# Kernel tuning notes

Hardware: AMD Instinct MI355X
Metric: run time of the kernel (lower is better)

Reference implementation:

```python
import jax, jax.numpy as jnp
import numpy as np

B, T = 32, 512
DA, DV = 1280, 768
D = DA + DV          # fused audio+video feature dim = 2048
DM = 256             # mamba d_model
L = 4                # n_layers
DI = 2 * DM          # d_inner (expand=2)
DS = 16              # d_state
DC = 4               # d_conv
R = DM // 16         # dt_rank = ceil(256/16)
H = 128              # attn-pool hidden
NC = 8               # emotion classes
EPS_TIN = 1e-5
EPS_LN = 1e-5


def _ln(x, g, b):
    mu = x.mean(-1, keepdims=True)
    v = ((x - mu) ** 2).mean(-1, keepdims=True)
    return (x - mu) / jnp.sqrt(v + EPS_LN) * g + b


def _mamba(u, in_w, cw, cb, xw, dtw, dtb, A_log, Dp, ow):
    # u: [B,T,DM] -> [B,T,DM]; Mamba(v1) selective scan, d_state=16, d_conv=4, expand=2
    xz = jnp.einsum('btd,ed->bte', u, in_w)            # [B,T,2*DI]
    x, z = xz[..., :DI], xz[..., DI:]
    xp = jnp.pad(x, ((0, 0), (DC - 1, 0), (0, 0)))     # causal depthwise conv1d
    xc = sum(xp[:, k:k + u.shape[1], :] * cw[:, k] for k in range(DC)) + cb
    x = jax.nn.silu(xc)
    dbc = jnp.einsum('btd,ed->bte', x, xw)             # [B,T,R+2*DS]
    dt = jax.nn.softplus(jnp.einsum('btr,dr->btd', dbc[..., :R], dtw) + dtb)
    Bm = dbc[..., R:R + DS]
    Cm = dbc[..., R + DS:]
    A = -jnp.exp(A_log)                                # [DI,DS]

    def step(h, inp):
        dt_t, B_t, C_t, x_t = inp                      # [B,DI],[B,DS],[B,DS],[B,DI]
        h = jnp.exp(dt_t[..., None] * A) * h + dt_t[..., None] * B_t[:, None, :] * x_t[..., None]
        return h, jnp.einsum('bds,bs->bd', h, C_t)

    h0 = jnp.zeros((u.shape[0], DI, DS), u.dtype)
    xs = (dt.swapaxes(0, 1), Bm.swapaxes(0, 1), Cm.swapaxes(0, 1), x.swapaxes(0, 1))
    _, ys = jax.lax.scan(step, h0, xs)
    y = ys.swapaxes(0, 1) + Dp * x
    y = y * jax.nn.silu(z)
    return jnp.einsum('bti,oi->bto', y, ow)


def _forward(x, tin_gamma, tin_beta, proj_w, proj_b, ln_g, ln_b, in_proj_w, conv_w, conv_b,
             x_proj_w, dt_proj_w, dt_proj_b, A_log, D_param, out_proj_w,
             out_ln_g, out_ln_b, res_scale, attn_w1, attn_b1, attn_w2, head_w, head_b, lengths):
    mask = jnp.arange(T)[None, :] < lengths[:, None]   # [B,T]
    m = mask[..., None].astype(x.dtype)
    # FusedTIN: masked temporal instance norm + affine
    denom = jnp.maximum(lengths, 1).astype(x.dtype)[:, None, None]
    mean = (x * m).sum(1, keepdims=True) / denom
    var = (((x - mean) ** 2) * m).sum(1, keepdims=True) / denom
    xn = (x - mean) / jnp.sqrt(var + EPS_TIN) * m
    xn = (xn * tin_gamma + tin_beta) * m
    # MambaStack: proj_in + prenorm residual mamba blocks (dropout = eval identity)
    h = jnp.einsum('btd,md->btm', xn, proj_w) + proj_b
    for l in range(L):
        y = _mamba(_ln(h, ln_g[l], ln_b[l]), in_proj_w[l], conv_w[l], conv_b[l],
                   x_proj_w[l], dt_proj_w[l], dt_proj_b[l], A_log[l], D_param[l], out_proj_w[l])
        h = h + res_scale * y
    h = _ln(h, out_ln_g, out_ln_b)
    # MaskedAttnPool
    s = jnp.einsum('bth,oh->bto', jnp.tanh(jnp.einsum('btd,hd->bth', h, attn_w1) + attn_b1), attn_w2)[..., 0]
    logits = jnp.where(mask, s, -jnp.inf)
    alpha = jnp.nan_to_num(jax.nn.softmax(logits, axis=1)) * mask
    alpha = alpha / jnp.clip(alpha.sum(1, keepdims=True), 1e-9)
    ctx = (alpha[..., None] * h).sum(1)
    # classifier head
    return jnp.einsum('bd,cd->bc', ctx, head_w) + head_b


def setup_inputs() -> dict:
    key = jax.random.key(0)
    ks = jax.random.split(key, 16)
    s = 0.05
    inp = {}
    inp['x'] = jax.random.normal(ks[0], (B, T, D), jnp.float32)
    inp['lengths'] = jax.random.randint(ks[1], (B,), T // 4, T + 1)
    inp['tin_gamma'] = jnp.ones((D,), jnp.float32)
    inp['tin_beta'] = jnp.zeros((D,), jnp.float32)
    inp['proj_w'] = jax.random.normal(ks[2], (DM, D), jnp.float32) * s
    inp['proj_b'] = jnp.zeros((DM,), jnp.float32)
    inp['ln_g'] = jnp.ones((L, DM), jnp.float32)
    inp['ln_b'] = jnp.zeros((L, DM), jnp.float32)
    inp['in_proj_w'] = jax.random.normal(ks[3], (L, 2 * DI, DM), jnp.float32) * s
    inp['conv_w'] = jax.random.normal(ks[4], (L, DI, DC), jnp.float32) * s
    inp['conv_b'] = jnp.zeros((L, DI), jnp.float32)
    inp['x_proj_w'] = jax.random.normal(ks[5], (L, R + 2 * DS, DI), jnp.float32) * s
    inp['dt_proj_w'] = jax.random.normal(ks[6], (L, DI, R), jnp.float32) * s
    inp['dt_proj_b'] = jnp.full((L, DI), -3.0, jnp.float32) + jax.random.normal(ks[7], (L, DI), jnp.float32) * 0.1
    inp['A_log'] = jnp.log(jnp.broadcast_to(jnp.arange(1, DS + 1, dtype=jnp.float32), (L, DI, DS)) + 0.0)
    inp['D_param'] = jnp.ones((L, DI), jnp.float32)
    inp['out_proj_w'] = jax.random.normal(ks[8], (L, DM, DI), jnp.float32) * s
    inp['out_ln_g'] = jnp.ones((DM,), jnp.float32)
    inp['out_ln_b'] = jnp.zeros((DM,), jnp.float32)
    inp['res_scale'] = jnp.asarray(0.1, jnp.float32)
    inp['attn_w1'] = jax.random.normal(ks[9], (H, DM), jnp.float32) * s
    inp['attn_b1'] = jnp.zeros((H,), jnp.float32)
    inp['attn_w2'] = jax.random.normal(ks[10], (1, H), jnp.float32) * s
    inp['head_w'] = jax.random.normal(ks[11], (NC, DM), jnp.float32) * s
    inp['head_b'] = jnp.zeros((NC,), jnp.float32)
    return inp


def reference(x, tin_gamma, tin_beta, proj_w, proj_b, ln_g, ln_b, in_proj_w, conv_w, conv_b,
              x_proj_w, dt_proj_w, dt_proj_b, A_log, D_param, out_proj_w,
              out_ln_g, out_ln_b, res_scale, attn_w1, attn_b1, attn_w2, head_w, head_b, lengths):
    return _forward(x, tin_gamma, tin_beta, proj_w, proj_b, ln_g, ln_b, in_proj_w, conv_w, conv_b,
                    x_proj_w, dt_proj_w, dt_proj_b, A_log, D_param, out_proj_w,
                    out_ln_g, out_ln_b, res_scale, attn_w1, attn_b1, attn_w2, head_w, head_b, lengths)
```

## Files before the change

kernel.cpp:

```cpp
#include <hip/hip_runtime.h>

#define NB 32
#define NT 512
#define ND 2048
#define NDM 256
#define NDI 512
#define NDS 16
#define NR 16
#define NH 128
#define NNC 8
#define NL 4
#define NM (NB*NT)

typedef __attribute__((ext_vector_type(8))) short short8;
typedef __attribute__((ext_vector_type(4))) float floatx4;

__device__ __forceinline__ unsigned short f2bf_rn(float f) {
    unsigned u = __builtin_bit_cast(unsigned, f);
    u += 0x7FFFu + ((u >> 16) & 1u);
    return (unsigned short)(u >> 16);
}
__device__ __forceinline__ void cvt8(const float* v, short8& h8, short8& l8) {
#pragma unroll
    for (int q = 0; q < 8; ++q) {
        unsigned short hb = f2bf_rn(v[q]);
        float hf = __builtin_bit_cast(float, (unsigned)hb << 16);
        h8[q] = (short)hb;
        l8[q] = (short)f2bf_rn(v[q] - hf);
    }
}
__device__ __forceinline__ float quad_sum(float v) {
    int i = __builtin_bit_cast(int, v);
    int j = __builtin_amdgcn_update_dpp(0, i, 0xB1, 0xF, 0xF, true);
    v += __builtin_bit_cast(float, j);
    i = __builtin_bit_cast(int, v);
    j = __builtin_amdgcn_update_dpp(0, i, 0x4E, 0xF, 0xF, true);
    v += __builtin_bit_cast(float, j);
    return v;
}

__global__ __launch_bounds__(256) void tin_stats_k(
    const float* __restrict__ x, const int* __restrict__ lengths,
    float* __restrict__ mean, float* __restrict__ rstd)
{
    __shared__ float rs_[4][64];
    __shared__ float rq_[4][64];
    const int b = blockIdx.x >> 5;
    const int d0 = (blockIdx.x & 31) << 6;
    const int dl = threadIdx.x & 63;
    const int strip = threadIdx.x >> 6;
    const int len = lengths[b];
    const int d = d0 + dl;
    float s = 0.f, q = 0.f;
    for (int t = strip; t < len; t += 4) {
        float v = x[((size_t)(b*NT + t))*ND + d];
        s += v; q += v*v;
    }
    rs_[strip][dl] = s; rq_[strip][dl] = q;
    __syncthreads();
    if (threadIdx.x < 64) {
        float S = rs_[0][dl]+rs_[1][dl]+rs_[2][dl]+rs_[3][dl];
        float Q = rq_[0][dl]+rq_[1][dl]+rq_[2][dl]+rq_[3][dl];
        float inv = 1.f / (float)(len < 1 ? 1 : len);
        float mu = S * inv;
        float var = Q * inv - mu*mu;
        mean[b*ND + d] = mu;
        rstd[b*ND + d] = rsqrtf(var + 1e-5f);
    }
}

#define SLN 264
__global__ __launch_bounds__(256) void tin_norm_k(
    const float* __restrict__ x, const int* __restrict__ lengths,
    const float* __restrict__ mean, const float* __restrict__ rstd,
    const float* __restrict__ g, const float* __restrict__ be,
    short* __restrict__ Oh, short* __restrict__ Ol)
{
    __shared__ float sT[16][SLN];
    const int tid = threadIdx.x;
    const int row = tid >> 4, c = tid & 15;
    const int m = blockIdx.x*16 + row;
    const int b = m >> 9, t = m & (NT-1);
    const int len = lengths[b];
    const int kg0 = blockIdx.y*256 + c*16;
    if (t >= len) {
#pragma unroll
        for (int i = 0; i < 16; ++i) sT[row][c*16 + i] = 0.f;
    } else {
#pragma unroll
        for (int qq = 0; qq < 4; ++qq) {
            const int kg = kg0 + qq*4;
            float4 v = *(const float4*)(x + (size_t)m*ND + kg);
            float4 mn = *(const float4*)(mean + b*ND + kg);
            float4 rr = *(const float4*)(rstd + b*ND + kg);
            float4 gg = *(const float4*)(g + kg);
            float4 bb = *(const float4*)(be + kg);
            sT[row][c*16+qq*4+0] = (v.x-mn.x)*rr.x*gg.x + bb.x;
            sT[row][c*16+qq*4+1] = (v.y-mn.y)*rr.y*gg.y + bb.y;
            sT[row][c*16+qq*4+2] = (v.z-mn.z)*rr.z*gg.z + bb.z;
            sT[row][c*16+qq*4+3] = (v.w-mn.w)*rr.w*gg.w + bb.w;
        }
    }
    __syncthreads();
#pragma unroll
    for (int q = 0; q < 2; ++q) {
        const int slot = tid + 256*q;
        const int tile = slot >> 6, ln2 = slot & 63;
        const int mr = ln2 & 15, kc = ln2 >> 4;
        float v[8];
        *(float4*)&v[0] = *(const float4*)&sT[mr][tile*32 + kc*8];
        *(float4*)&v[4] = *(const float4*)&sT[mr][tile*32 + kc*8 + 4];
        short8 h8, l8; cvt8(v, h8, l8);
        const size_t off = ((size_t)blockIdx.x*64 + blockIdx.y*8 + tile)*512 + ln2*8;
        *(short8*)(Oh + off) = h8;
        *(short8*)(Ol + off) = l8;
    }
}

__global__ __launch_bounds__(256) void wconv_k(
    const float* __restrict__ W, short* __restrict__ Oh, short* __restrict__ Ol,
    int K, int nmod, int nvalid)
{
    __shared__ float sT[16][SLN];
    const int tid = threadIdx.x;
    const int row = tid >> 4, c = tid & 15;
    const int n = blockIdx.x*16 + row;
    const int rr = n % nmod;
    const int kg0 = blockIdx.y*256 + c*16;
    if (rr >= nvalid) {
#pragma unroll
        for (int i = 0; i < 16; ++i) sT[row][c*16 + i] = 0.f;
    } else {
        const int src = (n/nmod)*nvalid + rr;
#pragma unroll
        for (int qq = 0; qq < 4; ++qq) {
            float4 v = *(const float4*)(W + (size_t)src*K + kg0 + qq*4);
            *(float4*)&sT[row][c*16+qq*4] = v;
        }
    }
    __syncthreads();
#pragma unroll
    for (int q = 0; q < 2; ++q) {
        const int slot = tid + 256*q;
        const int tile = slot >> 6, ln2 = slot & 63;
        const int mr = ln2 & 15, kc = ln2 >> 4;
        float v[8];
        *(float4*)&v[0] = *(const float4*)&sT[mr][tile*32 + kc*8];
        *(float4*)&v[4] = *(const float4*)&sT[mr][tile*32 + kc*8 + 4];
        short8 h8, l8; cvt8(v, h8, l8);
        const size_t off = ((size_t)blockIdx.x*(K>>5) + blockIdx.y*8 + tile)*512 + ln2*8;
        *(short8*)(Oh + off) = h8;
        *(short8*)(Ol + off) = l8;
    }
}

template<int MSUB, int NSUB, int EPI>
__global__ __launch_bounds__(256) void mgemm_k(
    const short* __restrict__ Ah, const short* __restrict__ Al,
    const short* __restrict__ Bh, const short* __restrict__ Bl,
    const float* __restrict__ bias, float* __restrict__ C,
    int ldc, int Nvalid, int K, const float* __restrict__ rsp)
{
    __shared__ __align__(16) short lds[(MSUB+NSUB)*1024];
    short* As_h = lds;
    short* As_l = lds + MSUB*512;
    short* Bs_h = lds + MSUB*1024;
    short* Bs_l = lds + MSUB*1024 + NSUB*512;
    const int tid = threadIdx.x, lane = tid & 63, w = tid >> 6;
    const int m0t = blockIdx.x * MSUB;
    const int n0t = blockIdx.y * NSUB;
    const int Ktiles = K >> 5;
    constexpr int MI = MSUB/2, NI = NSUB/2;
    constexpr int ASG = MSUB/4, BSG = NSUB/4;
    const int wm = w >> 1, wn = w & 1;

    floatx4 acc[MI][NI] = {};
    short8 rah[ASG], ral[ASG], rbh[BSG], rbl[BSG];

#pragma unroll
    for (int u = 0; u < ASG; ++u) {
        const size_t off = ((size_t)(m0t + w*ASG + u)*Ktiles)*512 + lane*8;
        rah[u] = *(const short8*)(Ah + off); ral[u] = *(const short8*)(Al + off);
    }
#pragma unroll
    for (int u = 0; u < BSG; ++u) {
        const size_t off = ((size_t)(n0t + w*BSG + u)*Ktiles)*512 + lane*8;
        rbh[u] = *(const short8*)(Bh + off); rbl[u] = *(const short8*)(Bl + off);
    }

    for (int kb = 0; kb < Ktiles; ++kb) {
        __syncthreads();
#pragma unroll
        for (int u = 0; u < ASG; ++u) {
            const int sub = w*ASG + u;
            *(short8*)&As_h[sub*512 + lane*8] = rah[u];
            *(short8*)&As_l[sub*512 + lane*8] = ral[u];
        }
#pragma unroll
        for (int u = 0; u < BSG; ++u) {
            const int sub = w*BSG + u;
            *(short8*)&Bs_h[sub*512 + lane*8] = rbh[u];
            *(short8*)&Bs_l[sub*512 + lane*8] = rbl[u];
        }
        __syncthreads();
        if (kb + 1 < Ktiles) {
#pragma unroll
            for (int u = 0; u < ASG; ++u) {
                const size_t off = ((size_t)(m0t + w*ASG + u)*Ktiles + kb + 1)*512 + lane*8;
                rah[u] = *(const short8*)(Ah + off); ral[u] = *(const short8*)(Al + off);
            }
#pragma unroll
            for (int u = 0; u < BSG; ++u) {
                const size_t off = ((size_t)(n0t + w*BSG + u)*Ktiles + kb + 1)*512 + lane*8;
                rbh[u] = *(const short8*)(Bh + off); rbl[u] = *(const short8*)(Bl + off);
            }
        }
        short8 fah[MI], fal[MI], fbh[NI], fbl[NI];
#pragma unroll
        for (int i = 0; i < MI; ++i) {
            const int sub = wm*MI + i;
            fah[i] = *(const short8*)&As_h[sub*512 + lane*8];
            fal[i] = *(const short8*)&As_l[sub*512 + lane*8];
        }
#pragma unroll
        for (int j = 0; j < NI; ++j) {
            const int sub = wn*NI + j;
            fbh[j] = *(const short8*)&Bs_h[sub*512 + lane*8];
            fbl[j] = *(const short8*)&Bs_l[sub*512 + lane*8];
        }
#pragma unroll
        for (int i = 0; i < MI; ++i)
#pragma unroll
            for (int j = 0; j < NI; ++j) {
                acc[i][j] = __builtin_amdgcn_mfma_f32_16x16x32_bf16(fah[i], fbh[j], acc[i][j], 0, 0, 0);
                acc[i][j] = __builtin_amdgcn_mfma_f32_16x16x32_bf16(fah[i], fbl[j], acc[i][j], 0, 0, 0);
                acc[i][j] = __builtin_amdgcn_mfma_f32_16x16x32_bf16(fal[i], fbh[j], acc[i][j], 0, 0, 0);
            }
    }

    const float rs = (EPI == 1) ? rsp[0] : 0.f;
    const int lc = lane >> 4, col = lane & 15;
#pragma unroll
    for (int j = 0; j < NI; ++j) {
        const int n = (n0t + wn*NI + j)*16 + col;
        if (n < Nvalid) {
            const float bv = (EPI != 1 && bias) ? bias[n] : 0.f;
#pragma unroll
            for (int i = 0; i < MI; ++i) {
                const int mb = (m0t + wm*MI + i)*16 + lc*4;
#pragma unroll
                for (int r = 0; r < 4; ++r) {
                    float v = acc[i][j][r];
                    float* cp = C + (size_t)(mb + r)*ldc + n;
                    if (EPI == 0)      *cp = v + bv;
                    else if (EPI == 1) *cp = fmaf(rs, v, *cp);
                    else               *cp = tanhf(v + bv);
                }
            }
        }
    }
}

template<int WF32>
__global__ __launch_bounds__(256) void ln_blk_k(
    const float* __restrict__ in, const float* __restrict__ g,
    const float* __restrict__ b,
    short* __restrict__ Oh, short* __restrict__ Ol, float* __restrict__ o32)
{
    __shared__ float sT[16][SLN];
    const int tid = threadIdx.x;
    const int row = tid >> 4, c = tid & 15;
    const int m = blockIdx.x*16 + row;
    float v[16];
#pragma unroll
    for (int qq = 0; qq < 4; ++qq)
        *(float4*)&v[qq*4] = *(const float4*)(in + (size_t)m*NDM + c*16 + qq*4);
    float s = 0.f, q = 0.f;
#pragma unroll
    for (int i = 0; i < 16; ++i) { s += v[i]; q += v[i]*v[i]; }
#pragma unroll
    for (int o = 8; o; o >>= 1) { s += __shfl_xor(s, o); q += __shfl_xor(q, o); }
    const float mu = s * (1.f/NDM);
    const float r = rsqrtf(q*(1.f/NDM) - mu*mu + 1e-5f);
#pragma unroll
    for (int i = 0; i < 16; ++i) {
        const int kg = c*16 + i;
        v[i] = (v[i]-mu)*r*g[kg] + b[kg];
        sT[row][kg] = v[i];
    }
    if (WF32) {
#pragma unroll
        for (int qq = 0; qq < 4; ++qq)
            *(float4*)(o32 + (size_t)m*NDM + c*16 + qq*4) = *(const float4*)&v[qq*4];
    }
    __syncthreads();
#pragma unroll
    for (int qv = 0; qv < 2; ++qv) {
        const int slot = tid + 256*qv;
        const int tile = slot >> 6, ln2 = slot & 63;
        const int mr = ln2 & 15, kc = ln2 >> 4;
        float vv[8];
        *(float4*)&vv[0] = *(const float4*)&sT[mr][tile*32 + kc*8];
        *(float4*)&vv[4] = *(const float4*)&sT[mr][tile*32 + kc*8 + 4];
        short8 h8, l8; cvt8(vv, h8, l8);
        const size_t off = ((size_t)blockIdx.x*8 + tile)*512 + ln2*8;
        *(short8*)(Oh + off) = h8;
        *(short8*)(Ol + off) = l8;
    }
}

#define SCV 520
__global__ __launch_bounds__(256) void conv_blk_k(
    const float* __restrict__ xz, const float* __restrict__ cw,
    const float* __restrict__ cb, float* __restrict__ xc32,
    short* __restrict__ Oh, short* __restrict__ Ol)
{
    __shared__ float sT[16][SCV];
    const int tid = threadIdx.x;
    const int row = tid >> 4, cg = tid & 15;
    const int m = blockIdx.x*16 + row;
    const int t = m & (NT-1);
#pragma unroll
    for (int grp = 0; grp < 4; ++grp) {
        const int ch = cg*32 + grp*8;
        float a[8];
        *(float4*)&a[0] = *(const float4*)(cb + ch);
        *(float4*)&a[4] = *(const float4*)(cb + ch + 4);
        float4 wv[8];
#pragma unroll
        for (int i = 0; i < 8; ++i) wv[i] = *(const float4*)(cw + (ch+i)*4);
#pragma unroll
        for (int kk = 0; kk < 4; ++kk) {
            if (t - 3 + kk >= 0) {
                const float* xp = xz + (size_t)(m-3+kk)*(2*NDI) + ch;
                float xv[8];
                *(float4*)&xv[0] = *(const float4*)xp;
                *(float4*)&xv[4] = *(const float4*)(xp + 4);
                const float tap[8] = {
                    kk==0?wv[0].x:kk==1?wv[0].y:kk==2?wv[0].z:wv[0].w,
                    kk==0?wv[1].x:kk==1?wv[1].y:kk==2?wv[1].z:wv[1].w,
                    kk==0?wv[2].x:kk==1?wv[2].y:kk==2?wv[2].z:wv[2].w,
                    kk==0?wv[3].x:kk==1?wv[3].y:kk==2?wv[3].z:wv[3].w,
                    kk==0?wv[4].x:kk==1?wv[4].y:kk==2?wv[4].z:wv[4].w,
                    kk==0?wv[5].x:kk==1?wv[5].y:kk==2?wv[5].z:wv[5].w,
                    kk==0?wv[6].x:kk==1?wv[6].y:kk==2?wv[6].z:wv[6].w,
                    kk==0?wv[7].x:kk==1?wv[7].y:kk==2?wv[7].z:wv[7].w};
#pragma unroll
                for (int i = 0; i < 8; ++i) a[i] = fmaf(xv[i], tap[i], a[i]);
            }
        }
#pragma unroll
        for (int i = 0; i < 8; ++i) a[i] = a[i] / (1.f + __expf(-a[i]));
        *(float4*)&sT[row][ch] = *(const float4*)&a[0];
        *(float4*)&sT[row][ch+4] = *(const float4*)&a[4];
        *(float4*)(xc32 + (size_t)m*NDI + ch) = *(const float4*)&a[0];
        *(float4*)(xc32 + (size_t)m*NDI + ch + 4) = *(const float4*)&a[4];
    }
    __syncthreads();
#pragma unroll
    for (int q = 0; q < 4; ++q) {
        const int slot = tid + 256*q;
        const int tile = slot >> 6, ln2 = slot & 63;
        const int mr = ln2 & 15, kc = ln2 >> 4;
        float vv[8];
        *(float4*)&vv[0] = *(const float4*)&sT[mr][tile*32 + kc*8];
        *(float4*)&vv[4] = *(const float4*)&sT[mr][tile*32 + kc*8 + 4];
        short8 h8, l8; cvt8(vv, h8, l8);
        const size_t off = ((size_t)blockIdx.x*16 + tile)*512 + ln2*8;
        *(short8*)(Oh + off) = h8;
        *(short8*)(Ol + off) = l8;
    }
}

__global__ __launch_bounds__(256) void dt_k(
    const float* __restrict__ dbc, const float* __restrict__ dtw,
    const float* __restrict__ dtb, float* __restrict__ dt)
{
    const int m = blockIdx.x;
    const float* rsrc = dbc + (size_t)m*48;
    float rv[16];
#pragma unroll
    for (int i = 0; i < 16; ++i) rv[i] = rsrc[i];
#pragma unroll
    for (int hh = 0; hh < 2; ++hh) {
        const int d = hh*256 + threadIdx.x;
        const float* wr = dtw + d*16;
        float a = dtb[d];
#pragma unroll
        for (int i = 0; i < 16; ++i) a = fmaf(rv[i], wr[i], a);
        dt[(size_t)m*NDI + d] = (a > 20.f) ? a : log1pf(__expf(a));
    }
}

__global__ __launch_bounds__(256) void scan_k(
    const float* __restrict__ dbc, const float* __restrict__ dtp,
    const float* __restrict__ xcp, const float* __restrict__ xz,
    const float* __restrict__ Alog, const float* __restrict__ Dp,
    short* __restrict__ Yh, short* __restrict__ Yl)
{
    __shared__ float sBC[64][32];
    __shared__ float sDt[64][68];
    __shared__ float sX[64][68];
    __shared__ float sY[64][68];
    const int tid = threadIdx.x;
    const int w = tid >> 6, lane = tid & 63;
    const int dl = lane >> 2, sg = lane & 3;
    const int b = blockIdx.x >> 3;
    const int d0 = (blockIdx.x & 7) << 6;
    const int dloc = w*16 + dl;
    const int d = d0 + dloc;
    float ar[4];
    {
        float4 al4 = *(const float4*)(Alog + d*NDS + sg*4);
        ar[0] = -__expf(al4.x); ar[1] = -__expf(al4.y);
        ar[2] = -__expf(al4.z); ar[3] = -__expf(al4.w);
    }
    const float Dpv = Dp[d];
    float hr[4] = {0.f, 0.f, 0.f, 0.f};
    const int mbase = b*NT;
    const int srow = tid >> 2, sq = (tid & 3) << 3;
    const int tr = tid >> 2, qq = tid & 3;

    for (int c0 = 0; c0 < NT; c0 += 64) {
        __syncthreads();
        {
            const float* dp_ = dbc + (size_t)(mbase + c0 + srow)*48 + 16 + sq;
            *(float4*)&sBC[srow][sq]   = *(const float4*)dp_;
            *(float4*)&sBC[srow][sq+4] = *(const float4*)(dp_ + 4);
        }
        {
            const float* dsrc = dtp + (size_t)(mbase + c0 + tr)*NDI + d0 + qq*16;
            const float* xsrc = xcp + (size_t)(mbase + c0 + tr)*NDI + d0 + qq*16;
#pragma unroll
            for (int i = 0; i < 4; ++i) {
                float4 dv = *(const float4*)(dsrc + i*4);
                float4 xv = *(const float4*)(xsrc + i*4);
                const int dd = qq*16 + i*4;
                sDt[dd+0][tr]=dv.x; sDt[dd+1][tr]=dv.y; sDt[dd+2][tr]=dv.z; sDt[dd+3][tr]=dv.w;
                sX[dd+0][tr]=xv.x;  sX[dd+1][tr]=xv.y;  sX[dd+2][tr]=xv.z;  sX[dd+3][tr]=xv.w;
            }
        }
        __syncthreads();
        float4 Bt[2][4], Ct[2][4], dt4[2], x4[2];
#pragma unroll
        for (int i = 0; i < 4; ++i) {
            Bt[0][i] = *(const float4*)&sBC[i][sg*4];
            Ct[0][i] = *(const float4*)&sBC[i][16 + sg*4];
        }
        dt4[0] = *(const float4*)&sDt[dloc][0];
        x4[0]  = *(const float4*)&sX[dloc][0];
#pragma unroll
        for (int g = 0; g < 16; ++g) {
            const int cur = g & 1, nxt = cur ^ 1;
            if (g < 15) {
                const int t4 = (g+1)*4;
#pragma unroll
                for (int i = 0; i < 4; ++i) {
                    Bt[nxt][i] = *(const float4*)&sBC[t4+i][sg*4];
                    Ct[nxt][i] = *(const float4*)&sBC[t4+i][16 + sg*4];
                }
                dt4[nxt] = *(const float4*)&sDt[dloc][t4];
                x4[nxt]  = *(const float4*)&sX[dloc][t4];
            }
#pragma unroll
            for (int i = 0; i < 4; ++i) {
                const float dtv = (i==0)?dt4[cur].x:(i==1)?dt4[cur].y:(i==2)?dt4[cur].z:dt4[cur].w;
                const float xv  = (i==0)?x4[cur].x:(i==1)?x4[cur].y:(i==2)?x4[cur].z:x4[cur].w;
                const float4 Bv = Bt[cur][i];
                const float4 Cv = Ct[cur][i];
                const float dbx = dtv * xv;
                float pa0 = __expf(dtv*ar[0]);
                float pa1 = __expf(dtv*ar[1]);
                float pa2 = __expf(dtv*ar[2]);
                float pa3 = __expf(dtv*ar[3]);
                hr[0] = fmaf(pa0, hr[0], dbx*Bv.x);
                hr[1] = fmaf(pa1, hr[1], dbx*Bv.y);
                hr[2] = fmaf(pa2, hr[2], dbx*Bv.z);
                hr[3] = fmaf(pa3, hr[3], dbx*Bv.w);
                float cp = hr[0]*Cv.x;
                cp = fmaf(hr[1], Cv.y, cp);
                cp = fmaf(hr[2], Cv.z, cp);
                cp = fmaf(hr[3], Cv.w, cp);
                cp = quad_sum(cp);
                if (sg == 0) sY[g*4 + i][dloc] = fmaf(Dpv, xv, cp);
            }
        }
        __syncthreads();
#pragma unroll
        for (int q = 0; q < 2; ++q) {
            const int slot = tid + 256*q;
            const int tile = slot >> 6, ln2 = slot & 63;
            const int tm = tile >> 1, tk = tile & 1;
            const int mr = ln2 & 15, kc = ln2 >> 4;
            const int m = mbase + c0 + tm*16 + mr;
            const int kd = d0 + tk*32 + kc*8;
            float yv[8];
            *(float4*)&yv[0] = *(const float4*)&sY[tm*16 + mr][tk*32 + kc*8];
            *(float4*)&yv[4] = *(const float4*)&sY[tm*16 + mr][tk*32 + kc*8 + 4];
            float zv[8];
            *(float4*)&zv[0] = *(const float4*)(xz + (size_t)m*(2*NDI) + NDI + kd);
            *(float4*)&zv[4] = *(const float4*)(xz + (size_t)m*(2*NDI) + NDI + kd + 4);
#pragma unroll
            for (int i = 0; i < 8; ++i)
                yv[i] *= zv[i] / (1.f + __expf(-zv[i]));
            short8 h8, l8; cvt8(yv, h8, l8);
            const size_t off = ((size_t)(m>>4)*16 + (kd>>5))*512 + ln2*8;
            *(short8*)(Yh + off) = h8;
            *(short8*)(Yl + off) = l8;
        }
    }
}

__global__ __launch_bounds__(64) void score_k(
    const float* __restrict__ t1, const float* __restrict__ w2,
    float* __restrict__ sout)
{
    const int m = blockIdx.x;
    const int lane = threadIdx.x;
    float v = t1[(size_t)m*NH + lane]*w2[lane]
            + t1[(size_t)m*NH + 64 + lane]*w2[64 + lane];
#pragma unroll
    for (int o = 32; o; o >>= 1) v += __shfl_xor(v, o);
    if (lane == 0) sout[m] = v;
}

__global__ __launch_bounds__(256) void pool_k(
    const float* __restrict__ sbuf, const float* __restrict__ u,
    const int* __restrict__ lengths, float* __restrict__ ctx)
{
    __shared__ float al[NT];
    __shared__ float red[256];
    const int b = blockIdx.x;
    const int tid = threadIdx.x;
    const int len = lengths[b];
    float mx = -3.4e38f;
    for (int t = tid; t < len; t += 256) mx = fmaxf(mx, sbuf[b*NT + t]);
    red[tid] = mx; __syncthreads();
    for (int o = 128; o; o >>= 1) { if (tid < o) red[tid] = fmaxf(red[tid], red[tid+o]); __syncthreads(); }
    mx = red[0];
    __syncthreads();
    float sm = 0.f;
    for (int t = tid; t < len; t += 256) {
        float e = __expf(sbuf[b*NT + t] - mx);
        al[t] = e; sm += e;
    }
    red[tid] = sm; __syncthreads();
    for (int o = 128; o; o >>= 1) { if (tid < o) red[tid] += red[tid+o]; __syncthreads(); }
    const float rZ = 1.f / red[0];
    float acc = 0.f;
    const float* up = u + (size_t)b*NT*NDM + tid;
    for (int t = 0; t < len; ++t) acc = fmaf(al[t], up[(size_t)t*NDM], acc);
    ctx[b*NDM + tid] = acc * rZ;
}

__global__ __launch_bounds__(64) void head_k(
    const float* __restrict__ ctx, const float* __restrict__ hw,
    const float* __restrict__ hb, float* __restrict__ o)
{
    const int b = blockIdx.x;
    const int lane = threadIdx.x;
    const float4 c4 = *(const float4*)(ctx + b*NDM + lane*4);
#pragma unroll
    for (int c = 0; c < NNC; ++c) {
        const float4 w4 = *(const float4*)(hw + c*NDM + lane*4);
        float v = c4.x*w4.x + c4.y*w4.y + c4.z*w4.z + c4.w*w4.w;
#pragma unroll
        for (int off = 32; off; off >>= 1) v += __shfl_xor(v, off);
        if (lane == 0) o[b*NNC + c] = v + hb[c];
    }
}

extern "C" void kernel_launch(void* const* d_in, const int* in_sizes, int n_in,
                              void* d_out, int out_size, void* d_ws, size_t ws_size,
                              hipStream_t stream)
{
    (void)in_sizes; (void)n_in; (void)out_size; (void)ws_size;
    const float* x         = (const float*)d_in[0];
    const int*   lengths   = (const int*)  d_in[1];
    const float* tin_gamma = (const float*)d_in[2];
    const float* tin_beta  = (const float*)d_in[3];
    const float* proj_w    = (const float*)d_in[4];
    const float* proj_b    = (const float*)d_in[5];
    const float* ln_g      = (const float*)d_in[6];
    const float* ln_b      = (const float*)d_in[7];
    const float* in_proj_w = (const float*)d_in[8];
    const float* conv_w    = (const float*)d_in[9];
    const float* conv_b    = (const float*)d_in[10];
    const float* x_proj_w  = (const float*)d_in[11];
    const float* dt_proj_w = (const float*)d_in[12];
    const float* dt_proj_b = (const float*)d_in[13];
    const float* A_log     = (const float*)d_in[14];
    const float* D_param   = (const float*)d_in[15];
    const float* out_proj_w= (const float*)d_in[16];
    const float* out_ln_g  = (const float*)d_in[17];
    const float* out_ln_b  = (const float*)d_in[18];
    const float* res_scale = (const float*)d_in[19];
    const float* attn_w1   = (const float*)d_in[20];
    const float* attn_b1   = (const float*)d_in[21];
    const float* attn_w2   = (const float*)d_in[22];
    const float* head_w    = (const float*)d_in[23];
    const float* head_b    = (const float*)d_in[24];
    float* out = (float*)d_out;

    float* ws = (float*)d_ws;
    float* mean   = ws;
    float* rstd   = mean + 65536;
    float* hbuf   = rstd + 65536;
    float* ubuf32 = hbuf + (size_t)NM*NDM;
    float* dbc    = ubuf32 + (size_t)NM*NDM;
    float* t1     = dbc + (size_t)NM*48;
    float* sbuf   = t1 + (size_t)NM*NH;
    float* ctx    = sbuf + NM;
    float* fend   = ctx + NB*NDM;
    short* ublk_h = (short*)fend;
    short* ublk_l = ublk_h + (size_t)NM*NDM;
    short* xcb_h  = ublk_l + (size_t)NM*NDM;
    short* xcb_l  = xcb_h + (size_t)NM*NDI;
    short* yq_h   = xcb_l + (size_t)NM*NDI;
    short* yq_l   = yq_h + (size_t)NM*NDI;
    short* pw_h   = yq_l + (size_t)NM*NDI;
    short* pw_l   = pw_h + (size_t)256*2048;
    short* iw_h   = pw_l + (size_t)256*2048;
    short* iw_l   = iw_h + (size_t)4*1024*256;
    short* xw_h   = iw_l + (size_t)4*1024*256;
    short* xw_l   = xw_h + (size_t)4*64*512;
    short* ow_h   = xw_l + (size_t)4*64*512;
    short* ow_l   = ow_h + (size_t)4*256*512;
    short* aw_h   = ow_l + (size_t)4*256*512;
    short* aw_l   = aw_h + (size_t)128*256;
    float* over   = (float*)(aw_l + (size_t)128*256);
    short* xn_h   = (short*)over;
    short* xn_l   = xn_h + (size_t)NM*ND;
    float* xz     = over;
    float* xc32   = over + (size_t)NM*2*NDI;
    float* dtb_   = xc32 + (size_t)NM*NDI;

    const dim3 blk(256);

    wconv_k<<<dim3(16, 8), blk, 0, stream>>>(proj_w, pw_h, pw_l, 2048, 1<<28, 1<<28);
    wconv_k<<<dim3(256, 1), blk, 0, stream>>>(in_proj_w, iw_h, iw_l, 256, 1<<28, 1<<28);
    wconv_k<<<dim3(16, 2), blk, 0, stream>>>(x_proj_w, xw_h, xw_l, 512, 64, 48);
    wconv_k<<<dim3(64, 2), blk, 0, stream>>>(out_proj_w, ow_h, ow_l, 512, 1<<28, 1<<28);
    wconv_k<<<dim3(8, 1), blk, 0, stream>>>(attn_w1, aw_h, aw_l, 256, 1<<28, 1<<28);

    tin_stats_k<<<dim3(NB*32), blk, 0, stream>>>(x, lengths, mean, rstd);
    tin_norm_k<<<dim3(NM/16, 8), blk, 0, stream>>>(x, lengths, mean, rstd,
        tin_gamma, tin_beta, xn_h, xn_l);
    mgemm_k<4,8,0><<<dim3(256, 2), blk, 0, stream>>>(
        xn_h, xn_l, pw_h, pw_l, proj_b, hbuf, NDM, NDM, 2048, nullptr);

    for (int l = 0; l < NL; ++l) {
        ln_blk_k<0><<<dim3(NM/16), blk, 0, stream>>>(
            hbuf, ln_g + l*NDM, ln_b + l*NDM, ublk_h, ublk_l, nullptr);
        mgemm_k<8,8,0><<<dim3(128, 8), blk, 0, stream>>>(
            ublk_h, ublk_l, iw_h + (size_t)l*1024*256, iw_l + (size_t)l*1024*256,
            nullptr, xz, 2*NDI, 2*NDI, NDM, nullptr);
        conv_blk_k<<<dim3(NM/16), blk, 0, stream>>>(
            xz, conv_w + (size_t)l*NDI*4, conv_b + (size_t)l*NDI, xc32, xcb_h, xcb_l);
        mgemm_k<4,4,0><<<dim3(256, 1), blk, 0, stream>>>(
            xcb_h, xcb_l, xw_h + (size_t)l*64*512, xw_l + (size_t)l*64*512,
            nullptr, dbc, 48, 48, 512, nullptr);
        dt_k<<<dim3(NM), blk, 0, stream>>>(
            dbc, dt_proj_w + (size_t)l*NDI*NR, dt_proj_b + (size_t)l*NDI, dtb_);
        scan_k<<<dim3(NB*8), blk, 0, stream>>>(
            dbc, dtb_, xc32, xz, A_log + (size_t)l*NDI*NDS, D_param + (size_t)l*NDI,
            yq_h, yq_l);
        mgemm_k<4,8,1><<<dim3(256, 2), blk, 0, stream>>>(
            yq_h, yq_l, ow_h + (size_t)l*256*512, ow_l + (size_t)l*256*512,
            nullptr, hbuf, NDM, NDM, 512, res_scale);
    }

    ln_blk_k<1><<<dim3(NM/16), blk, 0, stream>>>(
        hbuf, out_ln_g, out_ln_b, ublk_h, ublk_l, ubuf32);
    mgemm_k<4,8,2><<<dim3(256, 1), blk, 0, stream>>>(
        ublk_h, ublk_l, aw_h, aw_l, attn_b1, t1, NH, NH, 256, nullptr);
    score_k<<<dim3(NM), dim3(64), 0, stream>>>(t1, attn_w2, sbuf);
    pool_k<<<dim3(NB), blk, 0, stream>>>(sbuf, ubuf32, lengths, ctx);
    head_k<<<dim3(NB), dim3(64), 0, stream>>>(ctx, head_w, head_b, out);
}
```

Measured before the change: 1.501 ms.

## Add split-K with atomic accumulation and direct global-to-LDS loads in GEMM

The GEMM kernel gains a split-K mode. Blocks take a slice of the K tiles along grid z and accumulate into a zero-initialised output with atomicAdd, which raises the block count for the projection, x_proj and out_proj GEMMs. Register-staged prefetching is replaced by global_load_lds copies straight into shared memory, with an extra barrier per K step and no software double buffering. The attention GEMM tile is also reshaped to 4x4 with two column blocks. The risks are atomic traffic, the added memset launches, nondeterministic summation order, and lost load/compute overlap.

```diff
diff --git a/kernel.cpp b/kernel.cpp
--- a/kernel.cpp
+++ b/kernel.cpp
@@ -37,6 +37,11 @@
     j = __builtin_amdgcn_update_dpp(0, i, 0x4E, 0xF, 0xF, true);
     v += __builtin_bit_cast(float, j);
     return v;
+}
+__device__ __forceinline__ void glds16(const short* g, short* lds_base) {
+    __builtin_amdgcn_global_load_lds(
+        (const __attribute__((address_space(1))) void*)g,
+        (__attribute__((address_space(3))) void*)lds_base, 16, 0, 0);
 }
 
 __global__ __launch_bounds__(256) void tin_stats_k(
@@ -154,7 +159,7 @@
     }
 }
 
-template<int MSUB, int NSUB, int EPI>
+template<int MSUB, int NSUB, int EPI, int ATOMIC>
 __global__ __launch_bounds__(256) void mgemm_k(
     const short* __restrict__ Ah, const short* __restrict__ Al,
     const short* __restrict__ Bh, const short* __restrict__ Bl,
@@ -170,51 +175,31 @@
     const int m0t = blockIdx.x * MSUB;
     const int n0t = blockIdx.y * NSUB;
     const int Ktiles = K >> 5;
+    const int kslice = Ktiles / (int)gridDim.z;
+    const int kt0 = blockIdx.z * kslice;
     constexpr int MI = MSUB/2, NI = NSUB/2;
     constexpr int ASG = MSUB/4, BSG = NSUB/4;
     const int wm = w >> 1, wn = w & 1;
 
     floatx4 acc[MI][NI] = {};
-    short8 rah[ASG], ral[ASG], rbh[BSG], rbl[BSG];
-
-#pragma unroll
-    for (int u = 0; u < ASG; ++u) {
-        const size_t off = ((size_t)(m0t + w*ASG + u)*Ktiles)*512 + lane*8;
-        rah[u] = *(const short8*)(Ah + off); ral[u] = *(const short8*)(Al + off);
-    }
-#pragma unroll
-    for (int u = 0; u < BSG; ++u) {
-        const size_t off = ((size_t)(n0t + w*BSG + u)*Ktiles)*512 + lane*8;
-        rbh[u] = *(const short8*)(Bh + off); rbl[u] = *(const short8*)(Bl + off);
-    }
-
-    for (int kb = 0; kb < Ktiles; ++kb) {
-        __syncthreads();
+
+    for (int kk = 0; kk < kslice; ++kk) {
+        const int kb = kt0 + kk;
 #pragma unroll
         for (int u = 0; u < ASG; ++u) {
             const int sub = w*ASG + u;
-            *(short8*)&As_h[sub*512 + lane*8] = rah[u];
-            *(short8*)&As_l[sub*512 + lane*8] = ral[u];
+            const size_t off = ((size_t)(m0t + sub)*Ktiles + kb)*512 + lane*8;
+            glds16(Ah + off, &As_h[sub*512]);
+            glds16(Al + off, &As_l[sub*512]);
         }
 #pragma unroll
         for (int u = 0; u < BSG; ++u) {
             const int sub = w*BSG + u;
-            *(short8*)&Bs_h[sub*512 + lane*8] = rbh[u];
-            *(short8*)&Bs_l[sub*512 + lane*8] = rbl[u];
+            const size_t off = ((size_t)(n0t + sub)*Ktiles + kb)*512 + lane*8;
+            glds16(Bh + off, &Bs_h[sub*512]);
+            glds16(Bl + off, &Bs_l[sub*512]);
         }
         __syncthreads();
-        if (kb + 1 < Ktiles) {
-#pragma unroll
-            for (int u = 0; u < ASG; ++u) {
-                const size_t off = ((size_t)(m0t + w*ASG + u)*Ktiles + kb + 1)*512 + lane*8;
-                rah[u] = *(const short8*)(Ah + off); ral[u] = *(const short8*)(Al + off);
-            }
-#pragma unroll
-            for (int u = 0; u < BSG; ++u) {
-                const size_t off = ((size_t)(n0t + w*BSG + u)*Ktiles + kb + 1)*512 + lane*8;
-                rbh[u] = *(const short8*)(Bh + off); rbl[u] = *(const short8*)(Bl + off);
-            }
-        }
         short8 fah[MI], fal[MI], fbh[NI], fbl[NI];
 #pragma unroll
         for (int i = 0; i < MI; ++i) {
@@ -236,15 +221,17 @@
                 acc[i][j] = __builtin_amdgcn_mfma_f32_16x16x32_bf16(fah[i], fbl[j], acc[i][j], 0, 0, 0);
                 acc[i][j] = __builtin_amdgcn_mfma_f32_16x16x32_bf16(fal[i], fbh[j], acc[i][j], 0, 0, 0);
             }
+        __syncthreads();
     }
 
     const float rs = (EPI == 1) ? rsp[0] : 0.f;
     const int lc = lane >> 4, col = lane & 15;
+    const bool addb = (EPI != 1) && bias && (!ATOMIC || blockIdx.z == 0);
 #pragma unroll
     for (int j = 0; j < NI; ++j) {
         const int n = (n0t + wn*NI + j)*16 + col;
         if (n < Nvalid) {
-            const float bv = (EPI != 1 && bias) ? bias[n] : 0.f;
+            const float bv = addb ? bias[n] : 0.f;
 #pragma unroll
             for (int i = 0; i < MI; ++i) {
                 const int mb = (m0t + wm*MI + i)*16 + lc*4;
@@ -252,9 +239,14 @@
                 for (int r = 0; r < 4; ++r) {
                     float v = acc[i][j][r];
                     float* cp = C + (size_t)(mb + r)*ldc + n;
-                    if (EPI == 0)      *cp = v + bv;
-                    else if (EPI == 1) *cp = fmaf(rs, v, *cp);
-                    else               *cp = tanhf(v + bv);
+                    if (ATOMIC) {
+                        if (EPI == 1) atomicAdd(cp, rs*v);
+                        else          atomicAdd(cp, v + bv);
+                    } else {
+                        if (EPI == 0)      *cp = v + bv;
+                        else if (EPI == 1) *cp = fmaf(rs, v, *cp);
+                        else               *cp = tanhf(v + bv);
+                    }
                 }
             }
         }
@@ -646,18 +638,20 @@
     tin_stats_k<<<dim3(NB*32), blk, 0, stream>>>(x, lengths, mean, rstd);
     tin_norm_k<<<dim3(NM/16, 8), blk, 0, stream>>>(x, lengths, mean, rstd,
         tin_gamma, tin_beta, xn_h, xn_l);
-    mgemm_k<4,8,0><<<dim3(256, 2), blk, 0, stream>>>(
+    hipMemsetAsync(hbuf, 0, (size_t)NM*NDM*sizeof(float), stream);
+    mgemm_k<4,8,0,1><<<dim3(256, 2, 4), blk, 0, stream>>>(
         xn_h, xn_l, pw_h, pw_l, proj_b, hbuf, NDM, NDM, 2048, nullptr);
 
     for (int l = 0; l < NL; ++l) {
         ln_blk_k<0><<<dim3(NM/16), blk, 0, stream>>>(
             hbuf, ln_g + l*NDM, ln_b + l*NDM, ublk_h, ublk_l, nullptr);
-        mgemm_k<8,8,0><<<dim3(128, 8), blk, 0, stream>>>(
+        mgemm_k<8,8,0,0><<<dim3(128, 8, 1), blk, 0, stream>>>(
             ublk_h, ublk_l, iw_h + (size_t)l*1024*256, iw_l + (size_t)l*1024*256,
             nullptr, xz, 2*NDI, 2*NDI, NDM, nullptr);
         conv_blk_k<<<dim3(NM/16), blk, 0, stream>>>(
             xz, conv_w + (size_t)l*NDI*4, conv_b + (size_t)l*NDI, xc32, xcb_h, xcb_l);
-        mgemm_k<4,4,0><<<dim3(256, 1), blk, 0, stream>>>(
+        hipMemsetAsync(dbc, 0, (size_t)NM*48*sizeof(float), stream);
+        mgemm_k<4,4,0,1><<<dim3(256, 1, 2), blk, 0, stream>>>(
             xcb_h, xcb_l, xw_h + (size_t)l*64*512, xw_l + (size_t)l*64*512,
             nullptr, dbc, 48, 48, 512, nullptr);
         dt_k<<<dim3(NM), blk, 0, stream>>>(
@@ -665,14 +659,14 @@
         scan_k<<<dim3(NB*8), blk, 0, stream>>>(
             dbc, dtb_, xc32, xz, A_log + (size_t)l*NDI*NDS, D_param + (size_t)l*NDI,
             yq_h, yq_l);
-        mgemm_k<4,8,1><<<dim3(256, 2), blk, 0, stream>>>(
+        mgemm_k<4,8,1,1><<<dim3(256, 2, 2), blk, 0, stream>>>(
             yq_h, yq_l, ow_h + (size_t)l*256*512, ow_l + (size_t)l*256*512,
             nullptr, hbuf, NDM, NDM, 512, res_scale);
     }
 
     ln_blk_k<1><<<dim3(NM/16), blk, 0, stream>>>(
         hbuf, out_ln_g, out_ln_b, ublk_h, ublk_l, ubuf32);
-    mgemm_k<4,8,2><<<dim3(256, 1), blk, 0, stream>>>(
+    mgemm_k<4,4,2,0><<<dim3(256, 2, 1), blk, 0, stream>>>(
         ublk_h, ublk_l, aw_h, aw_l, attn_b1, t1, NH, NH, 256, nullptr);
     score_k<<<dim3(NM), dim3(64), 0, stream>>>(t1, attn_w2, sbuf);
     pool_k<<<dim3(NB), blk, 0, stream>>>(sbuf, ubuf32, lengths, ctx);
```

Result: slower. 1.584 ms (+5.5%).
